# Optimization experiments

Measured on AMD Instinct MI355X. Metric: run time of the kernel, lower is better.

The kernel has to match this reference:

```python
import jax, jax.numpy as jnp
import numpy as np

H = 128
L = 3
N = 100000
E = 1600000
G = 1024
OUT = 10
MAX_LEVEL = 1000
MAX_THOUGHTS = 5000
N_CATE = 5
BN_EPS = 1e-5


def _make_pe(n_pos, h):
    pos = np.arange(n_pos, dtype=np.float32)[:, None]
    div = np.exp(np.arange(0, h, 2, dtype=np.float32) * (-np.log(10000.0) / h))
    pe = np.zeros((n_pos, h), dtype=np.float32)
    pe[:, 0::2] = np.sin(pos * div)
    pe[:, 1::2] = np.cos(pos * div)
    return jnp.asarray(pe)


def setup_inputs() -> dict:
    key = jax.random.key(0)
    ks = jax.random.split(key, 16)
    s = 0.02
    inp = {
        "x": jax.random.randint(ks[0], (N, 3), 0, 5, dtype=jnp.int64 if jax.config.jax_enable_x64 else jnp.int32),
        "edge_index": jax.random.randint(ks[1], (2, E), 0, N),
        "batch": jnp.sort(jax.random.randint(ks[2], (N,), 0, G)),
        "num_graphs": G,
        "pe": _make_pe(MAX_THOUGHTS, H),
        "cate_emb": jax.random.normal(ks[3], (N_CATE, H), jnp.float32) * s,
        "level_emb": jax.random.normal(ks[4], (MAX_LEVEL, H), jnp.float32) * s,
        "conv_W1": jax.random.normal(ks[5], (L, H, H), jnp.float32) * s,
        "conv_b1": jnp.zeros((L, H), jnp.float32),
        "conv_g1": jnp.ones((L, H), jnp.float32),
        "conv_be1": jnp.zeros((L, H), jnp.float32),
        "conv_W2": jax.random.normal(ks[6], (L, H, H), jnp.float32) * s,
        "conv_b2": jnp.zeros((L, H), jnp.float32),
        "norm_g": jnp.ones((L, H), jnp.float32),
        "norm_be": jnp.zeros((L, H), jnp.float32),
        "gate_W1": jax.random.normal(ks[7], (H, H), jnp.float32) * s,
        "gate_b1": jnp.zeros((H,), jnp.float32),
        "gate_W2": jax.random.normal(ks[8], (H, 1), jnp.float32) * s,
        "gate_b2": jnp.zeros((1,), jnp.float32),
        "cls_W1": jax.random.normal(ks[9], (H, H), jnp.float32) * s,
        "cls_b1": jnp.zeros((H,), jnp.float32),
        "cls_g": jnp.ones((H,), jnp.float32),
        "cls_be": jnp.zeros((H,), jnp.float32),
        "cls_W2": jax.random.normal(ks[10], (H, OUT), jnp.float32) * s,
        "cls_b2": jnp.zeros((OUT,), jnp.float32),
    }
    return inp


def _bn(h, g, b):
    # BatchNorm1d, training mode: batch stats over the node/graph dim, biased var
    m = jnp.mean(h, axis=0)
    v = jnp.var(h, axis=0)
    return (h - m) * jax.lax.rsqrt(v + BN_EPS) * g + b


def reference(x, edge_index, batch, num_graphs, pe, cate_emb, level_emb,
              conv_W1, conv_b1, conv_g1, conv_be1, conv_W2, conv_b2,
              norm_g, norm_be, gate_W1, gate_b1, gate_W2, gate_b2,
              cls_W1, cls_b1, cls_g, cls_be, cls_W2, cls_b2):
    # NodeEncoder ('tree'): level + cate + sinusoidal thought PE
    level = jnp.clip(x[:, 0], 0, MAX_LEVEL - 1)
    cate = jnp.clip(x[:, 1], 0, N_CATE - 1)
    thought = jnp.clip(x[:, 2], 0, MAX_THOUGHTS - 1)
    h = cate_emb[cate] + level_emb[level] + pe[thought]  # [N, H]

    src, dst = edge_index[0], edge_index[1]
    n = h.shape[0]
    for i in range(L):
        # GINConv (eps=0): h_i <- MLP(h_i + sum_{j->i} h_j)
        agg = jax.ops.segment_sum(h[src], dst, num_segments=n)
        z = (h + agg) @ conv_W1[i] + conv_b1[i]
        z = jax.nn.relu(_bn(z, conv_g1[i], conv_be1[i]))
        z = z @ conv_W2[i] + conv_b2[i]
        h = jax.nn.relu(_bn(z, norm_g[i], norm_be[i]))

    # GlobalAttention pooling: per-graph softmax over gate scores
    gate = (jax.nn.relu(h @ gate_W1 + gate_b1) @ gate_W2 + gate_b2)[:, 0]  # [N]
    m = jax.ops.segment_max(gate, batch, num_segments=num_graphs)
    e = jnp.exp(gate - m[batch])
    s = jax.ops.segment_sum(e, batch, num_segments=num_graphs)
    alpha = e / s[batch]
    pooled = jax.ops.segment_sum(alpha[:, None] * h, batch, num_segments=num_graphs)  # [G, H]

    # classifier (dropout = 0)
    z = pooled @ cls_W1 + cls_b1
    z = jax.nn.relu(_bn(z, cls_g, cls_be))
    return z @ cls_W2 + cls_b2  # [G, OUT]
```

## Files before the change

kernel.cpp:

```cpp
#include <hip/hip_runtime.h>
#include <math.h>

#define HD 128

typedef __attribute__((ext_vector_type(8))) short bf16x8;
typedef __attribute__((ext_vector_type(8))) unsigned short us8;
typedef __attribute__((ext_vector_type(4))) unsigned short us4;
typedef __attribute__((ext_vector_type(4))) float f32x4;

__device__ __forceinline__ float bf2f(unsigned short u) {
  union { unsigned int i; float f; } v; v.i = ((unsigned int)u) << 16; return v.f;
}
__device__ __forceinline__ unsigned short f2bf(float f) {
  union { float f; unsigned int i; } v; v.f = f;
  unsigned int u = v.i;
  u += 0x7FFFu + ((u >> 16) & 1u);
  return (unsigned short)(u >> 16);
}

__global__ void zero_f(float* p, int n) {
  int i = blockIdx.x * blockDim.x + threadIdx.x;
  if (i < n) p[i] = 0.f;
}

__global__ void zero_int(int* p, int n) {
  int stride = gridDim.x * blockDim.x;
  for (int i = blockIdx.x * blockDim.x + threadIdx.x; i < n; i += stride) p[i] = 0;
}

__global__ void encode_kernel(const int* __restrict__ x, const float* __restrict__ pe,
                              const float* __restrict__ ce, const float* __restrict__ le,
                              float* __restrict__ h, unsigned short* __restrict__ hb, int n) {
  int total = n * HD;
  int stride = gridDim.x * blockDim.x;
  for (int idx = blockIdx.x * blockDim.x + threadIdx.x; idx < total; idx += stride) {
    int node = idx >> 7, c = idx & (HD - 1);
    int lv = x[node * 3 + 0]; lv = lv < 0 ? 0 : (lv > 999 ? 999 : lv);
    int ct = x[node * 3 + 1]; ct = ct < 0 ? 0 : (ct > 4 ? 4 : ct);
    int th = x[node * 3 + 2]; th = th < 0 ? 0 : (th > 4999 ? 4999 : th);
    float v = ce[ct * HD + c] + le[lv * HD + c] + pe[th * HD + c];
    h[idx] = v;
    hb[idx] = f2bf(v);
  }
}

__global__ void prep_w(const float* __restrict__ cW1, const float* __restrict__ cW2,
                       const float* __restrict__ gW1,
                       unsigned short* __restrict__ whi, unsigned short* __restrict__ wlo) {
  int m = blockIdx.x;
  const float* W = (m < 3) ? cW1 + (size_t)m * HD * HD
                 : (m < 6) ? cW2 + (size_t)(m - 3) * HD * HD : gW1;
  unsigned short* oh = whi + (size_t)m * HD * HD;
  unsigned short* ol = wlo + (size_t)m * HD * HD;
  for (int i = threadIdx.x; i < HD * HD; i += 256) {
    int j = i & 7;
    int l = (i >> 3) & 63;
    int p = i >> 9;
    int cg = p >> 2, k4 = p & 3;
    int c = cg * 16 + (l & 15);
    int k = (k4 * 4 + (l >> 4)) * 8 + j;
    float f = W[k * HD + c];
    unsigned short hh = f2bf(f);
    oh[i] = hh;
    ol[i] = f2bf(f - bf2f(hh));
  }
}


__global__ void hist_kernel(const int* __restrict__ ei, int* deg, int E, int Wwin) {
  int pass = blockIdx.x & 7;
  int b = blockIdx.x >> 3;
  int tstride = (gridDim.x >> 3) * blockDim.x;
  for (int e = b * blockDim.x + threadIdx.x; e < E; e += tstride) {
    int d = ei[E + e];
    if (d / Wwin == pass) atomicAdd(&deg[d], 1);
  }
}

#define SCAN_BS 1024
__global__ void scan1_kernel(const int* __restrict__ deg, int* __restrict__ off,
                             int* __restrict__ bsum, int n) {
  __shared__ int sh[256];
  int b = blockIdx.x, t = threadIdx.x;
  int base = b * SCAN_BS + t * 4;
  int v[4];
#pragma unroll
  for (int j = 0; j < 4; j++) v[j] = (base + j < n) ? deg[base + j] : 0;
  int s = v[0] + v[1] + v[2] + v[3];
  sh[t] = s;
  __syncthreads();
  for (int o = 1; o < 256; o <<= 1) {
    int x = (t >= o) ? sh[t - o] : 0;
    __syncthreads();
    sh[t] += x;
    __syncthreads();
  }
  int excl = sh[t] - s;
  if (t == 255) bsum[b] = sh[255];
  int run = excl;
#pragma unroll
  for (int j = 0; j < 4; j++) {
    if (base + j < n) off[base + j] = run;
    run += v[j];
  }
}

__global__ void scan2_kernel(int* bsum, int nb) {
  __shared__ int sh[128];
  int t = threadIdx.x;
  int v = (t < nb) ? bsum[t] : 0;
  sh[t] = v;
  __syncthreads();
  for (int o = 1; o < 128; o <<= 1) {
    int x = (t >= o) ? sh[t - o] : 0;
    __syncthreads();
    sh[t] += x;
    __syncthreads();
  }
  if (t < nb) bsum[t] = sh[t] - v;
}

__global__ void scan3_kernel(int* off, int* cursor, const int* __restrict__ bsum,
                             int n, int E) {
  int idx = blockIdx.x * blockDim.x + threadIdx.x;
  int stride = gridDim.x * blockDim.x;
  for (int i = idx; i < n; i += stride) {
    int v = off[i] + bsum[i >> 10];
    off[i] = v;
    cursor[i] = v;
  }
  if (idx == 0) off[n] = E;
}

__global__ void fill_kernel(const int* __restrict__ ei, int* cursor, int* csr_src,
                            int E, int Wwin) {
  int pass = blockIdx.x & 7;
  int b = blockIdx.x >> 3;
  int tstride = (gridDim.x >> 3) * blockDim.x;
  for (int e = b * blockDim.x + threadIdx.x; e < E; e += tstride) {
    int d = ei[E + e];
    if (d / Wwin == pass) {
      int pos = atomicAdd(&cursor[d], 1);
      csr_src[pos] = ei[e];
    }
  }
}

template<bool BN, bool STATS>
__global__ __launch_bounds__(512, 4)
void gemm_gather(const float* __restrict__ h, const unsigned short* __restrict__ hb,
                 const int* __restrict__ off,
                 const int* __restrict__ src, const float* __restrict__ ab,
                 const unsigned short* __restrict__ Whi,
                 const unsigned short* __restrict__ Wlo,
                 const float* __restrict__ bias, float* __restrict__ outf,
                 float* __restrict__ stat, int Nn) {
  __shared__ unsigned short XsH[128 * HD];
  __shared__ unsigned short XsL[128 * HD];
  __shared__ float red[2 * HD];
  int t = threadIdx.x;
  long rowbase = (long)blockIdx.x * 128;
  int grp = t >> 5, lane = t & 31;

  float4 a4, b4;
  if (BN) {
    a4 = *(const float4*)(ab + lane * 4);
    b4 = *(const float4*)(ab + HD + lane * 4);
  }
#define APPLY_BN(v) if (BN) { \
    v.x = fmaxf(v.x * a4.x + b4.x, 0.f); \
    v.y = fmaxf(v.y * a4.y + b4.y, 0.f); \
    v.z = fmaxf(v.z * a4.z + b4.z, 0.f); \
    v.w = fmaxf(v.w * a4.w + b4.w, 0.f); }
#define UP4(wv) {bf2f(wv[0]), bf2f(wv[1]), bf2f(wv[2]), bf2f(wv[3])}

  for (int rr = 0; rr < 8; rr++) {
    int r = grp + rr * 16;
    long row = rowbase + r; if (row > Nn - 1) row = Nn - 1;
    int s0 = off[row], s1 = off[row + 1];
    float4 acc0 = *(const float4*)(h + row * HD + lane * 4);
    APPLY_BN(acc0);
    float4 acc1 = {0.f, 0.f, 0.f, 0.f};
    float4 acc2 = {0.f, 0.f, 0.f, 0.f};
    float4 acc3 = {0.f, 0.f, 0.f, 0.f};
    int e = s0;
    for (; e + 8 <= s1; e += 8) {
      int i0 = src[e], i1 = src[e + 1], i2 = src[e + 2], i3 = src[e + 3];
      int i4 = src[e + 4], i5 = src[e + 5], i6 = src[e + 6], i7 = src[e + 7];
      us4 w0 = *(const us4*)(hb + (size_t)i0 * HD + lane * 4);
      us4 w1 = *(const us4*)(hb + (size_t)i1 * HD + lane * 4);
      us4 w2 = *(const us4*)(hb + (size_t)i2 * HD + lane * 4);
      us4 w3 = *(const us4*)(hb + (size_t)i3 * HD + lane * 4);
      us4 w4 = *(const us4*)(hb + (size_t)i4 * HD + lane * 4);
      us4 w5 = *(const us4*)(hb + (size_t)i5 * HD + lane * 4);
      us4 w6 = *(const us4*)(hb + (size_t)i6 * HD + lane * 4);
      us4 w7 = *(const us4*)(hb + (size_t)i7 * HD + lane * 4);
      float4 v0 = UP4(w0), v1 = UP4(w1), v2 = UP4(w2), v3 = UP4(w3);
      float4 v4 = UP4(w4), v5 = UP4(w5), v6 = UP4(w6), v7 = UP4(w7);
      APPLY_BN(v0); APPLY_BN(v1); APPLY_BN(v2); APPLY_BN(v3);
      APPLY_BN(v4); APPLY_BN(v5); APPLY_BN(v6); APPLY_BN(v7);
      acc0.x += v0.x + v4.x; acc0.y += v0.y + v4.y; acc0.z += v0.z + v4.z; acc0.w += v0.w + v4.w;
      acc1.x += v1.x + v5.x; acc1.y += v1.y + v5.y; acc1.z += v1.z + v5.z; acc1.w += v1.w + v5.w;
      acc2.x += v2.x + v6.x; acc2.y += v2.y + v6.y; acc2.z += v2.z + v6.z; acc2.w += v2.w + v6.w;
      acc3.x += v3.x + v7.x; acc3.y += v3.y + v7.y; acc3.z += v3.z + v7.z; acc3.w += v3.w + v7.w;
    }
    for (; e < s1; e++) {
      int s = src[e];
      us4 wv = *(const us4*)(hb + (size_t)s * HD + lane * 4);
      float4 v = UP4(wv);
      APPLY_BN(v);
      acc0.x += v.x; acc0.y += v.y; acc0.z += v.z; acc0.w += v.w;
    }
    acc0.x += acc1.x + acc2.x + acc3.x;
    acc0.y += acc1.y + acc2.y + acc3.y;
    acc0.z += acc1.z + acc2.z + acc3.z;
    acc0.w += acc1.w + acc2.w + acc3.w;
    float f[4] = {acc0.x, acc0.y, acc0.z, acc0.w};
    us4 hi, lo;
#pragma unroll
    for (int j = 0; j < 4; j++) {
      unsigned short hh = f2bf(f[j]);
      hi[j] = hh;
      lo[j] = f2bf(f[j] - bf2f(hh));
    }
    int g8 = lane >> 1;
    int offl = r * HD + (((g8 ^ (r & 7)) << 3)) + (lane & 1) * 4;
    *(us4*)(XsH + offl) = hi;
    *(us4*)(XsL + offl) = lo;
  }
#undef APPLY_BN
#undef UP4
  if (STATS && t < 2 * HD) red[t] = 0.f;
  __syncthreads();

  int w = t >> 6, l = t & 63;
  int lr = l & 15, lg = l >> 4;

  f32x4 acc[8];
#pragma unroll
  for (int ct = 0; ct < 8; ct++) acc[ct] = (f32x4){0.f, 0.f, 0.f, 0.f};

  bf16x8 aH[4], aL[4];
  int arow = w * 16 + lr;
#pragma unroll
  for (int k4 = 0; k4 < 4; k4++) {
    int kg = k4 * 4 + lg;
    int offa = arow * HD + (((kg ^ (arow & 7)) << 3));
    aH[k4] = *(bf16x8*)(XsH + offa);
    aL[k4] = *(bf16x8*)(XsL + offa);
  }
#pragma unroll
  for (int ct = 0; ct < 8; ct++) {
#pragma unroll
    for (int k4 = 0; k4 < 4; k4++) {
      int bo = (((ct << 2) + k4) * 64 + l) * 8;
      bf16x8 bH = *(const bf16x8*)(Whi + bo);
      bf16x8 bL = *(const bf16x8*)(Wlo + bo);
      acc[ct] = __builtin_amdgcn_mfma_f32_16x16x32_bf16(aH[k4], bH, acc[ct], 0, 0, 0);
      acc[ct] = __builtin_amdgcn_mfma_f32_16x16x32_bf16(aH[k4], bL, acc[ct], 0, 0, 0);
      acc[ct] = __builtin_amdgcn_mfma_f32_16x16x32_bf16(aL[k4], bH, acc[ct], 0, 0, 0);
    }
  }

  float s[8], ss[8];
#pragma unroll
  for (int ct = 0; ct < 8; ct++) { s[ct] = 0.f; ss[ct] = 0.f; }
#pragma unroll
  for (int jj = 0; jj < 4; jj++) {
    long row = rowbase + w * 16 + lg * 4 + jj;
    bool ok = row < Nn;
#pragma unroll
    for (int ct = 0; ct < 8; ct++) {
      float v = acc[ct][jj] + bias[ct * 16 + lr];
      if (ok) {
        outf[row * HD + ct * 16 + lr] = v;
        if (STATS) { s[ct] += v; ss[ct] += v * v; }
      }
    }
  }
  if (STATS) {
#pragma unroll
    for (int ct = 0; ct < 8; ct++) {
      float sv = s[ct], sq = ss[ct];
      sv += __shfl_xor(sv, 16); sq += __shfl_xor(sq, 16);
      sv += __shfl_xor(sv, 32); sq += __shfl_xor(sq, 32);
      if (lg == 0) {
        atomicAdd(&red[ct * 16 + lr], sv);
        atomicAdd(&red[HD + ct * 16 + lr], sq);
      }
    }
    __syncthreads();
    float* st = stat + (blockIdx.x & 3) * 256;
    if (t < 2 * HD) atomicAdd(&st[t], red[t]);
  }
}

template<bool INBN, bool GATE, bool STATS>
__global__ __launch_bounds__(512, 8)
void gemm_split(const float* __restrict__ X, const unsigned short* __restrict__ Whi,
                const unsigned short* __restrict__ Wlo,
                const float* __restrict__ bias, const float* __restrict__ ab,
                const float* __restrict__ w2, float* __restrict__ outf,
                unsigned short* __restrict__ outb,
                float* __restrict__ gate, float* __restrict__ stat, int Nn) {
  __shared__ unsigned short XsH[64 * HD];
  __shared__ unsigned short XsL[64 * HD];
  __shared__ float red[2 * HD];
  __shared__ float gred[64];
  int t = threadIdx.x;
  long rowbase = (long)blockIdx.x * 64;

#pragma unroll
  for (int it = 0; it < 4; it++) {
    int i = (t + it * 512) * 4;
    int r = i >> 7, k = i & (HD - 1);
    long row = rowbase + r; if (row > Nn - 1) row = Nn - 1;
    float4 v = *(const float4*)(X + row * HD + k);
    float f[4] = {v.x, v.y, v.z, v.w};
    if (INBN) {
#pragma unroll
      for (int j = 0; j < 4; j++)
        f[j] = fmaxf(f[j] * ab[k + j] + ab[HD + k + j], 0.f);
    }
    us4 hi, lo;
#pragma unroll
    for (int j = 0; j < 4; j++) {
      unsigned short hh = f2bf(f[j]);
      hi[j] = hh;
      lo[j] = f2bf(f[j] - bf2f(hh));
    }
    int g = k >> 3;
    int off = r * HD + ((((g ^ (r & 7)) << 3)) | (k & 7));
    *(us4*)(XsH + off) = hi;
    *(us4*)(XsL + off) = lo;
  }
  if (STATS && t < 2 * HD) red[t] = 0.f;
  if (GATE && t < 64) gred[t] = 0.f;
  __syncthreads();

  int w = t >> 6, l = t & 63;
  int lr = l & 15, lg = l >> 4;
  int wr = w & 3, wc = w >> 2;

  f32x4 acc[4];
#pragma unroll
  for (int ct = 0; ct < 4; ct++) acc[ct] = (f32x4){0.f, 0.f, 0.f, 0.f};

  bf16x8 aH[4], aL[4];
  int arow = wr * 16 + lr;
#pragma unroll
  for (int k4 = 0; k4 < 4; k4++) {
    int kg = k4 * 4 + lg;
    int off = arow * HD + (((kg ^ (arow & 7)) << 3));
    aH[k4] = *(bf16x8*)(XsH + off);
    aL[k4] = *(bf16x8*)(XsL + off);
  }
#pragma unroll
  for (int ct = 0; ct < 4; ct++) {
    int cg = wc * 4 + ct;
#pragma unroll
    for (int k4 = 0; k4 < 4; k4++) {
      int bo = (((cg << 2) + k4) * 64 + l) * 8;
      bf16x8 bH = *(const bf16x8*)(Whi + bo);
      bf16x8 bL = *(const bf16x8*)(Wlo + bo);
      acc[ct] = __builtin_amdgcn_mfma_f32_16x16x32_bf16(aH[k4], bH, acc[ct], 0, 0, 0);
      acc[ct] = __builtin_amdgcn_mfma_f32_16x16x32_bf16(aH[k4], bL, acc[ct], 0, 0, 0);
      acc[ct] = __builtin_amdgcn_mfma_f32_16x16x32_bf16(aL[k4], bH, acc[ct], 0, 0, 0);
    }
  }

  if (GATE) {
#pragma unroll
    for (int jj = 0; jj < 4; jj++) {
      float p = 0.f;
#pragma unroll
      for (int ct = 0; ct < 4; ct++) {
        int col = (wc * 4 + ct) * 16 + lr;
        float v = fmaxf(acc[ct][jj] + bias[col], 0.f);
        p += v * w2[col];
      }
      p += __shfl_xor(p, 1);
      p += __shfl_xor(p, 2);
      p += __shfl_xor(p, 4);
      p += __shfl_xor(p, 8);
      if (lr == 0) atomicAdd(&gred[wr * 16 + lg * 4 + jj], p);
    }
    __syncthreads();
    if (t < 64 && rowbase + t < Nn) gate[rowbase + t] = gred[t];
  } else {
    float s[4], ss[4];
#pragma unroll
    for (int ct = 0; ct < 4; ct++) { s[ct] = 0.f; ss[ct] = 0.f; }
#pragma unroll
    for (int jj = 0; jj < 4; jj++) {
      long row = rowbase + wr * 16 + lg * 4 + jj;
      bool ok = row < Nn;
#pragma unroll
      for (int ct = 0; ct < 4; ct++) {
        int col = (wc * 4 + ct) * 16 + lr;
        float v = acc[ct][jj] + bias[col];
        if (ok) {
          outf[row * HD + col] = v;
          if (outb) outb[row * HD + col] = f2bf(v);
          if (STATS) { s[ct] += v; ss[ct] += v * v; }
        }
      }
    }
    if (STATS) {
#pragma unroll
      for (int ct = 0; ct < 4; ct++) {
        int col = (wc * 4 + ct) * 16 + lr;
        float sv = s[ct], sq = ss[ct];
        sv += __shfl_xor(sv, 16); sq += __shfl_xor(sq, 16);
        sv += __shfl_xor(sv, 32); sq += __shfl_xor(sq, 32);
        if (lg == 0) {
          atomicAdd(&red[col], sv);
          atomicAdd(&red[HD + col], sq);
        }
      }
      __syncthreads();
      float* st = stat + (blockIdx.x & 3) * 256;
      if (t < 2 * HD) atomicAdd(&st[t], red[t]);
    }
  }
}

__global__ void finalize_kernel(const float* __restrict__ stat, const float* __restrict__ g,
                                const float* __restrict__ be, float* ab, float inv_n) {
  int c = threadIdx.x;
  float s = stat[c] + stat[256 + c] + stat[512 + c] + stat[768 + c];
  float sq = stat[HD + c] + stat[256 + HD + c] + stat[512 + HD + c] + stat[768 + HD + c];
  float mean = s * inv_n;
  float var = sq * inv_n - mean * mean;
  float inv = rsqrtf(var + 1e-5f);
  float a = inv * g[c];
  ab[c] = a;
  ab[HD + c] = be[c] - mean * a;
}

__global__ void finalize1_kernel(const float* __restrict__ stat, const float* __restrict__ g,
                                 const float* __restrict__ be, float* ab, float inv_n) {
  int c = threadIdx.x;
  float mean = stat[c] * inv_n;
  float var = stat[HD + c] * inv_n - mean * mean;
  float inv = rsqrtf(var + 1e-5f);
  float a = inv * g[c];
  ab[c] = a;
  ab[HD + c] = be[c] - mean * a;
}

__global__ void bound_kernel(const int* __restrict__ batch, int* gs, int N, int G) {
  int i = blockIdx.x * blockDim.x + threadIdx.x;
  if (i >= N) return;
  int b = batch[i];
  int prev = (i == 0) ? -1 : batch[i - 1];
  for (int g = prev + 1; g <= b; g++) gs[g] = i;
  if (i == N - 1)
    for (int g = b + 1; g <= G; g++) gs[g] = N;
}

__global__ void fused_pool(const float* __restrict__ h, const float* __restrict__ gate,
                           const int* __restrict__ gs, const float* __restrict__ ab,
                           float* __restrict__ pooled) {
  int g = blockIdx.x;
  int t = threadIdx.x;
  int s0 = gs[g], s1 = gs[g + 1];
  if (s0 >= s1) { pooled[(size_t)g * HD + t] = 0.f; return; }
  __shared__ float red[HD];
  float m = -INFINITY;
  for (int i = s0 + t; i < s1; i += HD) m = fmaxf(m, gate[i]);
  red[t] = m;
  __syncthreads();
  for (int o = 64; o > 0; o >>= 1) {
    if (t < o) red[t] = fmaxf(red[t], red[t + o]);
    __syncthreads();
  }
  m = red[0];
  __syncthreads();
  float s = 0.f;
  for (int i = s0 + t; i < s1; i += HD) s += expf(gate[i] - m);
  red[t] = s;
  __syncthreads();
  for (int o = 64; o > 0; o >>= 1) {
    if (t < o) red[t] += red[t + o];
    __syncthreads();
  }
  float inv = 1.f / red[0];
  float a = ab[t], b = ab[HD + t];
  float acc = 0.f;
  int i = s0;
  for (; i + 4 <= s1; i += 4) {
    float al0 = expf(gate[i] - m);
    float al1 = expf(gate[i + 1] - m);
    float al2 = expf(gate[i + 2] - m);
    float al3 = expf(gate[i + 3] - m);
    float v0 = fmaxf(h[(size_t)(i + 0) * HD + t] * a + b, 0.f);
    float v1 = fmaxf(h[(size_t)(i + 1) * HD + t] * a + b, 0.f);
    float v2 = fmaxf(h[(size_t)(i + 2) * HD + t] * a + b, 0.f);
    float v3 = fmaxf(h[(size_t)(i + 3) * HD + t] * a + b, 0.f);
    acc += al0 * v0 + al1 * v1 + al2 * v2 + al3 * v3;
  }
  for (; i < s1; i++) {
    float al = expf(gate[i] - m);
    float v = fmaxf(h[(size_t)i * HD + t] * a + b, 0.f);
    acc += al * v;
  }
  pooled[(size_t)g * HD + t] = acc * inv;
}

__global__ __launch_bounds__(256, 4)
void gemm_f32(const float* __restrict__ X, const float* __restrict__ W,
              const float* __restrict__ bias, float* __restrict__ out, int Nn) {
  __shared__ float XsT[32][132];
  __shared__ float Ws[32][HD];
  int t = threadIdx.x;
  int r0 = (t >> 4) * 8;
  int c0 = (t & 15) * 8;
  long rowbase = (long)blockIdx.x * 128;

  float acc[8][8];
#pragma unroll
  for (int ci = 0; ci < 8; ci++) {
    float bv = bias[c0 + ci];
#pragma unroll
    for (int ri = 0; ri < 8; ri++) acc[ri][ci] = bv;
  }

  int sr = t >> 1;
  int hf = t & 1;
  long srow = rowbase + sr; if (srow > Nn - 1) srow = Nn - 1;
  const float* xrow = X + srow * HD;

  for (int k0 = 0; k0 < HD; k0 += 32) {
    __syncthreads();
#pragma unroll
    for (int j = 0; j < 4; j++) {
      int i = j * 1024 + t * 4;
      int kk = i >> 7, c = i & (HD - 1);
      *(float4*)&Ws[kk][c] = *(const float4*)&W[(size_t)(k0 + kk) * HD + c];
    }
#pragma unroll
    for (int j = 0; j < 4; j++) {
      int kc = k0 + hf * 16 + j * 4;
      float4 v = *(const float4*)&xrow[kc];
      int kl = hf * 16 + j * 4;
      XsT[kl + 0][sr] = v.x;
      XsT[kl + 1][sr] = v.y;
      XsT[kl + 2][sr] = v.z;
      XsT[kl + 3][sr] = v.w;
    }
    __syncthreads();
#pragma unroll 8
    for (int kk = 0; kk < 32; kk++) {
      float4 a0 = *(float4*)&XsT[kk][r0];
      float4 a1 = *(float4*)&XsT[kk][r0 + 4];
      float4 b0 = *(float4*)&Ws[kk][c0];
      float4 b1 = *(float4*)&Ws[kk][c0 + 4];
      float ar[8] = {a0.x, a0.y, a0.z, a0.w, a1.x, a1.y, a1.z, a1.w};
      float bc[8] = {b0.x, b0.y, b0.z, b0.w, b1.x, b1.y, b1.z, b1.w};
#pragma unroll
      for (int ri = 0; ri < 8; ri++)
#pragma unroll
        for (int ci = 0; ci < 8; ci++) acc[ri][ci] += ar[ri] * bc[ci];
    }
  }

#pragma unroll
  for (int ri = 0; ri < 8; ri++) {
    long row = rowbase + r0 + ri;
    if (row < Nn) {
      float4 o0 = {acc[ri][0], acc[ri][1], acc[ri][2], acc[ri][3]};
      float4 o1 = {acc[ri][4], acc[ri][5], acc[ri][6], acc[ri][7]};
      *(float4*)&out[row * HD + c0] = o0;
      *(float4*)&out[row * HD + c0 + 4] = o1;
    }
  }
}

__global__ void stats_f32(const float* __restrict__ z, float* stat, int n) {
  int c = threadIdx.x & (HD - 1);
  int rg = threadIdx.x >> 7;
  float s = 0.f, ss = 0.f;
  for (int r = blockIdx.x * 2 + rg; r < n; r += gridDim.x * 2) {
    float v = z[(size_t)r * HD + c];
    s += v; ss += v * v;
  }
  __shared__ float S[2][HD], SS[2][HD];
  S[rg][c] = s; SS[rg][c] = ss;
  __syncthreads();
  if (threadIdx.x < HD) {
    atomicAdd(&stat[c], S[0][c] + S[1][c]);
    atomicAdd(&stat[HD + c], SS[0][c] + SS[1][c]);
  }
}

__global__ void cls_out_kernel(const float* __restrict__ zc, const float* __restrict__ ab,
                               const float* __restrict__ W2, const float* __restrict__ b2,
                               float* out, int G) {
  int row = blockIdx.x;
  int t = threadIdx.x;
  float v0 = fmaxf(zc[(size_t)row * HD + t] * ab[t] + ab[HD + t], 0.f);
  float v1 = fmaxf(zc[(size_t)row * HD + 64 + t] * ab[64 + t] + ab[HD + 64 + t], 0.f);
  for (int o = 0; o < 10; o++) {
    float p = v0 * W2[t * 10 + o] + v1 * W2[(64 + t) * 10 + o];
#pragma unroll
    for (int s = 32; s > 0; s >>= 1) p += __shfl_down(p, s);
    if (t == 0) out[row * 10 + o] = p + b2[o];
  }
}

extern "C" void kernel_launch(void* const* d_in, const int* in_sizes, int n_in,
                              void* d_out, int out_size, void* d_ws, size_t ws_size,
                              hipStream_t stream) {
  const int* x     = (const int*)d_in[0];
  const int* ei    = (const int*)d_in[1];
  const int* batch = (const int*)d_in[2];
  const float* pe  = (const float*)d_in[4];
  const float* ce  = (const float*)d_in[5];
  const float* le  = (const float*)d_in[6];
  const float* cW1 = (const float*)d_in[7];
  const float* cb1 = (const float*)d_in[8];
  const float* cg1 = (const float*)d_in[9];
  const float* cbe1= (const float*)d_in[10];
  const float* cW2 = (const float*)d_in[11];
  const float* cb2 = (const float*)d_in[12];
  const float* ngm = (const float*)d_in[13];
  const float* nbe = (const float*)d_in[14];
  const float* gW1 = (const float*)d_in[15];
  const float* gb1 = (const float*)d_in[16];
  const float* gW2 = (const float*)d_in[17];
  const float* clW1= (const float*)d_in[19];
  const float* clb1= (const float*)d_in[20];
  const float* clg = (const float*)d_in[21];
  const float* clbe= (const float*)d_in[22];
  const float* clW2= (const float*)d_in[23];
  const float* clb2= (const float*)d_in[24];

  int N = in_sizes[2];
  int E = in_sizes[1] / 2;
  int G = out_size / 10;

  float* buf0   = (float*)d_ws;
  float* buf1   = buf0 + (size_t)N * HD;
  float* pooled = buf1 + (size_t)N * HD;
  float* gate   = pooled + (size_t)G * HD;
  float* zc     = gate + N;
  float* stats  = zc + (size_t)G * HD;
  float* ab     = stats + 7 * 1024;
  unsigned short* whi = (unsigned short*)(ab + 7 * 256);
  unsigned short* wlo = whi + 7 * HD * HD;
  unsigned short* hbb = wlo + 7 * HD * HD;
  int* csr_off  = (int*)(hbb + (size_t)N * HD);
  int* cursor   = csr_off + (N + 1);
  int* bsum     = cursor + N;
  int* gs       = bsum + 128;
  int* csr_src  = gs + (G + 1);

  float* out = (float*)d_out;
  int gatherBlocks = (N + 127) / 128;
  int splitBlocks  = (N + 63) / 64;
  int Wwin = (N + 7) / 8;

  zero_f<<<28, 256, 0, stream>>>(stats, 7 * 1024);
  encode_kernel<<<2048, 256, 0, stream>>>(x, pe, ce, le, buf0, hbb, N);
  prep_w<<<7, 256, 0, stream>>>(cW1, cW2, gW1, whi, wlo);

  int nb = (N + SCAN_BS - 1) / SCAN_BS;
  zero_int<<<256, 256, 0, stream>>>(cursor, N);
  hist_kernel<<<2048, 256, 0, stream>>>(ei, cursor, E, Wwin);
  scan1_kernel<<<nb, 256, 0, stream>>>(cursor, csr_off, bsum, N);
  scan2_kernel<<<1, 128, 0, stream>>>(bsum, nb);
  scan3_kernel<<<256, 256, 0, stream>>>(csr_off, cursor, bsum, N, E);
  fill_kernel<<<2048, 256, 0, stream>>>(ei, cursor, csr_src, E, Wwin);
  bound_kernel<<<(N + 255) / 256, 256, 0, stream>>>(batch, gs, N, G);

  for (int l = 0; l < 3; l++) {
    float* abPrev = ab + (l - 1) * 512 + 256;
    if (l == 0)
      gemm_gather<false, true><<<gatherBlocks, 512, 0, stream>>>(
          buf0, hbb, csr_off, csr_src, nullptr,
          whi + (size_t)l * HD * HD, wlo + (size_t)l * HD * HD,
          cb1 + l * HD, buf1, stats + l * 2048, N);
    else
      gemm_gather<true, true><<<gatherBlocks, 512, 0, stream>>>(
          buf0, hbb, csr_off, csr_src, abPrev,
          whi + (size_t)l * HD * HD, wlo + (size_t)l * HD * HD,
          cb1 + l * HD, buf1, stats + l * 2048, N);
    finalize_kernel<<<1, 128, 0, stream>>>(stats + l * 2048, cg1 + l * HD, cbe1 + l * HD,
                                           ab + l * 512, 1.f / N);
    gemm_split<true, false, true><<<splitBlocks, 512, 0, stream>>>(
        buf1, whi + (size_t)(3 + l) * HD * HD, wlo + (size_t)(3 + l) * HD * HD,
        cb2 + l * HD, ab + l * 512, nullptr, buf0, (l < 2) ? hbb : nullptr,
        nullptr, stats + l * 2048 + 1024, N);
    finalize_kernel<<<1, 128, 0, stream>>>(stats + l * 2048 + 1024, ngm + l * HD, nbe + l * HD,
                                           ab + l * 512 + 256, 1.f / N);
  }

  const float* abFin = ab + 2 * 512 + 256;
  gemm_split<true, true, false><<<splitBlocks, 512, 0, stream>>>(
      buf0, whi + (size_t)6 * HD * HD, wlo + (size_t)6 * HD * HD,
      gb1, abFin, gW2, nullptr, nullptr, gate, nullptr, N);
  fused_pool<<<G, HD, 0, stream>>>(buf0, gate, gs, abFin, pooled);

  gemm_f32<<<(G + 127) / 128, 256, 0, stream>>>(pooled, clW1, clb1, zc, G);
  stats_f32<<<64, 256, 0, stream>>>(zc, stats + 6 * 1024, G);
  finalize1_kernel<<<1, 128, 0, stream>>>(stats + 6 * 1024, clg, clbe, ab + 6 * 256, 1.f / G);
  cls_out_kernel<<<G, 64, 0, stream>>>(zc, ab + 6 * 256, clW2, clb2, out, G);
}
```

Before: 774.3 us.

## Fold BatchNorm finalize into consumer kernels and shrink gather tile to 96 rows

Removes the separate single-block finalize kernels by having each consumer kernel (gather GEMM, split GEMM, pooling, classifier output) compute the BatchNorm scale and shift from the raw stats in its prologue. This saves seven tiny launches and their serialization gaps. Separately, the gather GEMM tile drops from 128 to 96 rows with launch bounds raised from 4 to 6 blocks, to cut LDS use and raise occupancy. Two of the eight waves now sit idle during the MFMA phase, and the stats math is repeated in every block.

```diff
diff --git a/kernel.cpp b/kernel.cpp
--- a/kernel.cpp
+++ b/kernel.cpp
@@ -4,7 +4,6 @@
 #define HD 128
 
 typedef __attribute__((ext_vector_type(8))) short bf16x8;
-typedef __attribute__((ext_vector_type(8))) unsigned short us8;
 typedef __attribute__((ext_vector_type(4))) unsigned short us4;
 typedef __attribute__((ext_vector_type(4))) float f32x4;
 
@@ -16,6 +15,18 @@
   unsigned int u = v.i;
   u += 0x7FFFu + ((u >> 16) & 1u);
   return (unsigned short)(u >> 16);
+}
+
+__device__ __forceinline__ void bn_ab(const float* __restrict__ st, const float* __restrict__ g,
+                                      const float* __restrict__ be, float inv_n, int c,
+                                      float& a, float& b) {
+  float s = st[c] + st[256 + c] + st[512 + c] + st[768 + c];
+  float sq = st[HD + c] + st[256 + HD + c] + st[512 + HD + c] + st[768 + HD + c];
+  float mean = s * inv_n;
+  float var = sq * inv_n - mean * mean;
+  float inv = rsqrtf(var + 1e-5f);
+  a = inv * g[c];
+  b = be[c] - mean * a;
 }
 
 __global__ void zero_f(float* p, int n) {
@@ -147,25 +158,37 @@
 }
 
 template<bool BN, bool STATS>
-__global__ __launch_bounds__(512, 4)
+__global__ __launch_bounds__(512, 6)
 void gemm_gather(const float* __restrict__ h, const unsigned short* __restrict__ hb,
-                 const int* __restrict__ off,
-                 const int* __restrict__ src, const float* __restrict__ ab,
+                 const int* __restrict__ off, const int* __restrict__ src,
+                 const float* __restrict__ statP, const float* __restrict__ gBN,
+                 const float* __restrict__ beBN, float inv_n,
                  const unsigned short* __restrict__ Whi,
                  const unsigned short* __restrict__ Wlo,
                  const float* __restrict__ bias, float* __restrict__ outf,
-                 float* __restrict__ stat, int Nn) {
-  __shared__ unsigned short XsH[128 * HD];
-  __shared__ unsigned short XsL[128 * HD];
+                 float* __restrict__ statOut, int Nn) {
+  __shared__ unsigned short XsH[96 * HD];
+  __shared__ unsigned short XsL[96 * HD];
   __shared__ float red[2 * HD];
+  __shared__ float abl[2 * HD];
   int t = threadIdx.x;
-  long rowbase = (long)blockIdx.x * 128;
+  long rowbase = (long)blockIdx.x * 96;
   int grp = t >> 5, lane = t & 31;
+
+  if (BN) {
+    if (t < HD) {
+      float a, b;
+      bn_ab(statP, gBN, beBN, inv_n, t, a, b);
+      abl[t] = a;
+      abl[HD + t] = b;
+    }
+    __syncthreads();
+  }
 
   float4 a4, b4;
   if (BN) {
-    a4 = *(const float4*)(ab + lane * 4);
-    b4 = *(const float4*)(ab + HD + lane * 4);
+    a4 = *(const float4*)(abl + lane * 4);
+    b4 = *(const float4*)(abl + HD + lane * 4);
   }
 #define APPLY_BN(v) if (BN) { \
     v.x = fmaxf(v.x * a4.x + b4.x, 0.f); \
@@ -174,7 +197,7 @@
     v.w = fmaxf(v.w * a4.w + b4.w, 0.f); }
 #define UP4(wv) {bf2f(wv[0]), bf2f(wv[1]), bf2f(wv[2]), bf2f(wv[3])}
 
-  for (int rr = 0; rr < 8; rr++) {
+  for (int rr = 0; rr < 6; rr++) {
     int r = grp + rr * 16;
     long row = rowbase + r; if (row > Nn - 1) row = Nn - 1;
     int s0 = off[row], s1 = off[row + 1];
@@ -236,61 +259,65 @@
   int w = t >> 6, l = t & 63;
   int lr = l & 15, lg = l >> 4;
 
-  f32x4 acc[8];
-#pragma unroll
-  for (int ct = 0; ct < 8; ct++) acc[ct] = (f32x4){0.f, 0.f, 0.f, 0.f};
-
-  bf16x8 aH[4], aL[4];
-  int arow = w * 16 + lr;
-#pragma unroll
-  for (int k4 = 0; k4 < 4; k4++) {
-    int kg = k4 * 4 + lg;
-    int offa = arow * HD + (((kg ^ (arow & 7)) << 3));
-    aH[k4] = *(bf16x8*)(XsH + offa);
-    aL[k4] = *(bf16x8*)(XsL + offa);
-  }
-#pragma unroll
-  for (int ct = 0; ct < 8; ct++) {
+  if (w < 6) {
+    f32x4 acc[8];
+#pragma unroll
+    for (int ct = 0; ct < 8; ct++) acc[ct] = (f32x4){0.f, 0.f, 0.f, 0.f};
+
+    bf16x8 aH[4], aL[4];
+    int arow = w * 16 + lr;
 #pragma unroll
     for (int k4 = 0; k4 < 4; k4++) {
-      int bo = (((ct << 2) + k4) * 64 + l) * 8;
-      bf16x8 bH = *(const bf16x8*)(Whi + bo);
-      bf16x8 bL = *(const bf16x8*)(Wlo + bo);
-      acc[ct] = __builtin_amdgcn_mfma_f32_16x16x32_bf16(aH[k4], bH, acc[ct], 0, 0, 0);
-      acc[ct] = __builtin_amdgcn_mfma_f32_16x16x32_bf16(aH[k4], bL, acc[ct], 0, 0, 0);
-      acc[ct] = __builtin_amdgcn_mfma_f32_16x16x32_bf16(aL[k4], bH, acc[ct], 0, 0, 0);
-    }
-  }
-
-  float s[8], ss[8];
-#pragma unroll
-  for (int ct = 0; ct < 8; ct++) { s[ct] = 0.f; ss[ct] = 0.f; }
-#pragma unroll
-  for (int jj = 0; jj < 4; jj++) {
-    long row = rowbase + w * 16 + lg * 4 + jj;
-    bool ok = row < Nn;
+      int kg = k4 * 4 + lg;
+      int offa = arow * HD + (((kg ^ (arow & 7)) << 3));
+      aH[k4] = *(bf16x8*)(XsH + offa);
+      aL[k4] = *(bf16x8*)(XsL + offa);
+    }
 #pragma unroll
     for (int ct = 0; ct < 8; ct++) {
-      float v = acc[ct][jj] + bias[ct * 16 + lr];
-      if (ok) {
-        outf[row * HD + ct * 16 + lr] = v;
-        if (STATS) { s[ct] += v; ss[ct] += v * v; }
+#pragma unroll
+      for (int k4 = 0; k4 < 4; k4++) {
+        int bo = (((ct << 2) + k4) * 64 + l) * 8;
+        bf16x8 bH = *(const bf16x8*)(Whi + bo);
+        bf16x8 bL = *(const bf16x8*)(Wlo + bo);
+        acc[ct] = __builtin_amdgcn_mfma_f32_16x16x32_bf16(aH[k4], bH, acc[ct], 0, 0, 0);
+        acc[ct] = __builtin_amdgcn_mfma_f32_16x16x32_bf16(aH[k4], bL, acc[ct], 0, 0, 0);
+        acc[ct] = __builtin_amdgcn_mfma_f32_16x16x32_bf16(aL[k4], bH, acc[ct], 0, 0, 0);
       }
     }
+
+    float s[8], ss[8];
+#pragma unroll
+    for (int ct = 0; ct < 8; ct++) { s[ct] = 0.f; ss[ct] = 0.f; }
+#pragma unroll
+    for (int jj = 0; jj < 4; jj++) {
+      long row = rowbase + w * 16 + lg * 4 + jj;
+      bool ok = row < Nn;
+#pragma unroll
+      for (int ct = 0; ct < 8; ct++) {
+        float v = acc[ct][jj] + bias[ct * 16 + lr];
+        if (ok) {
+          outf[row * HD + ct * 16 + lr] = v;
+          if (STATS) { s[ct] += v; ss[ct] += v * v; }
+        }
+      }
+    }
+    if (STATS) {
+#pragma unroll
+      for (int ct = 0; ct < 8; ct++) {
+        float sv = s[ct], sq = ss[ct];
+        sv += __shfl_xor(sv, 16); sq += __shfl_xor(sq, 16);
+        sv += __shfl_xor(sv, 32); sq += __shfl_xor(sq, 32);
+        if (lg == 0) {
+          atomicAdd(&red[ct * 16 + lr], sv);
+          atomicAdd(&red[HD + ct * 16 + lr], sq);
+        }
+      }
+    }
   }
   if (STATS) {
-#pragma unroll
-    for (int ct = 0; ct < 8; ct++) {
-      float sv = s[ct], sq = ss[ct];
-      sv += __shfl_xor(sv, 16); sq += __shfl_xor(sq, 16);
-      sv += __shfl_xor(sv, 32); sq += __shfl_xor(sq, 32);
-      if (lg == 0) {
-        atomicAdd(&red[ct * 16 + lr], sv);
-        atomicAdd(&red[HD + ct * 16 + lr], sq);
-      }
-    }
-    __syncthreads();
-    float* st = stat + (blockIdx.x & 3) * 256;
+    __syncthreads();
+    float* st = statOut + (blockIdx.x & 3) * 256;
     if (t < 2 * HD) atomicAdd(&st[t], red[t]);
   }
 }
@@ -299,16 +326,31 @@
 __global__ __launch_bounds__(512, 8)
 void gemm_split(const float* __restrict__ X, const unsigned short* __restrict__ Whi,
                 const unsigned short* __restrict__ Wlo,
-                const float* __restrict__ bias, const float* __restrict__ ab,
+                const float* __restrict__ bias,
+                const float* __restrict__ statP, const float* __restrict__ gBN,
+                const float* __restrict__ beBN, float inv_n,
                 const float* __restrict__ w2, float* __restrict__ outf,
                 unsigned short* __restrict__ outb,
-                float* __restrict__ gate, float* __restrict__ stat, int Nn) {
+                float* __restrict__ gate, float* __restrict__ statOut, int Nn) {
   __shared__ unsigned short XsH[64 * HD];
   __shared__ unsigned short XsL[64 * HD];
   __shared__ float red[2 * HD];
   __shared__ float gred[64];
+  __shared__ float abl[2 * HD];
   int t = threadIdx.x;
   long rowbase = (long)blockIdx.x * 64;
+
+  if (INBN) {
+    if (t < HD) {
+      float a, b;
+      bn_ab(statP, gBN, beBN, inv_n, t, a, b);
+      abl[t] = a;
+      abl[HD + t] = b;
+    }
+  }
+  if (STATS && t < 2 * HD) red[t] = 0.f;
+  if (GATE && t < 64) gred[t] = 0.f;
+  if (INBN) __syncthreads();
 
 #pragma unroll
   for (int it = 0; it < 4; it++) {
@@ -320,7 +362,7 @@
     if (INBN) {
 #pragma unroll
       for (int j = 0; j < 4; j++)
-        f[j] = fmaxf(f[j] * ab[k + j] + ab[HD + k + j], 0.f);
+        f[j] = fmaxf(f[j] * abl[k + j] + abl[HD + k + j], 0.f);
     }
     us4 hi, lo;
 #pragma unroll
@@ -334,8 +376,6 @@
     *(us4*)(XsH + off) = hi;
     *(us4*)(XsL + off) = lo;
   }
-  if (STATS && t < 2 * HD) red[t] = 0.f;
-  if (GATE && t < 64) gred[t] = 0.f;
   __syncthreads();
 
   int w = t >> 6, l = t & 63;
@@ -419,34 +459,10 @@
         }
       }
       __syncthreads();
-      float* st = stat + (blockIdx.x & 3) * 256;
+      float* st = statOut + (blockIdx.x & 3) * 256;
       if (t < 2 * HD) atomicAdd(&st[t], red[t]);
     }
   }
-}
-
-__global__ void finalize_kernel(const float* __restrict__ stat, const float* __restrict__ g,
-                                const float* __restrict__ be, float* ab, float inv_n) {
-  int c = threadIdx.x;
-  float s = stat[c] + stat[256 + c] + stat[512 + c] + stat[768 + c];
-  float sq = stat[HD + c] + stat[256 + HD + c] + stat[512 + HD + c] + stat[768 + HD + c];
-  float mean = s * inv_n;
-  float var = sq * inv_n - mean * mean;
-  float inv = rsqrtf(var + 1e-5f);
-  float a = inv * g[c];
-  ab[c] = a;
-  ab[HD + c] = be[c] - mean * a;
-}
-
-__global__ void finalize1_kernel(const float* __restrict__ stat, const float* __restrict__ g,
-                                 const float* __restrict__ be, float* ab, float inv_n) {
-  int c = threadIdx.x;
-  float mean = stat[c] * inv_n;
-  float var = stat[HD + c] * inv_n - mean * mean;
-  float inv = rsqrtf(var + 1e-5f);
-  float a = inv * g[c];
-  ab[c] = a;
-  ab[HD + c] = be[c] - mean * a;
 }
 
 __global__ void bound_kernel(const int* __restrict__ batch, int* gs, int N, int G) {
@@ -460,13 +476,17 @@
 }
 
 __global__ void fused_pool(const float* __restrict__ h, const float* __restrict__ gate,
-                           const int* __restrict__ gs, const float* __restrict__ ab,
+                           const int* __restrict__ gs,
+                           const float* __restrict__ statP, const float* __restrict__ gBN,
+                           const float* __restrict__ beBN, float inv_n,
                            float* __restrict__ pooled) {
   int g = blockIdx.x;
   int t = threadIdx.x;
   int s0 = gs[g], s1 = gs[g + 1];
   if (s0 >= s1) { pooled[(size_t)g * HD + t] = 0.f; return; }
   __shared__ float red[HD];
+  float a, b;
+  bn_ab(statP, gBN, beBN, inv_n, t, a, b);
   float m = -INFINITY;
   for (int i = s0 + t; i < s1; i += HD) m = fmaxf(m, gate[i]);
   red[t] = m;
@@ -486,7 +506,6 @@
     __syncthreads();
   }
   float inv = 1.f / red[0];
-  float a = ab[t], b = ab[HD + t];
   float acc = 0.f;
   int i = s0;
   for (; i + 4 <= s1; i += 4) {
@@ -594,13 +613,22 @@
   }
 }
 
-__global__ void cls_out_kernel(const float* __restrict__ zc, const float* __restrict__ ab,
-                               const float* __restrict__ W2, const float* __restrict__ b2,
-                               float* out, int G) {
+__global__ void cls_out_kernel(const float* __restrict__ zc, const float* __restrict__ stat,
+                               const float* __restrict__ g, const float* __restrict__ be,
+                               float inv_n, const float* __restrict__ W2,
+                               const float* __restrict__ b2, float* out, int G) {
   int row = blockIdx.x;
   int t = threadIdx.x;
-  float v0 = fmaxf(zc[(size_t)row * HD + t] * ab[t] + ab[HD + t], 0.f);
-  float v1 = fmaxf(zc[(size_t)row * HD + 64 + t] * ab[64 + t] + ab[HD + 64 + t], 0.f);
+  float mean0 = stat[t] * inv_n;
+  float var0 = stat[HD + t] * inv_n - mean0 * mean0;
+  float a0 = rsqrtf(var0 + 1e-5f) * g[t];
+  float b0 = be[t] - mean0 * a0;
+  float mean1 = stat[64 + t] * inv_n;
+  float var1 = stat[HD + 64 + t] * inv_n - mean1 * mean1;
+  float a1 = rsqrtf(var1 + 1e-5f) * g[64 + t];
+  float b1 = be[64 + t] - mean1 * a1;
+  float v0 = fmaxf(zc[(size_t)row * HD + t] * a0 + b0, 0.f);
+  float v1 = fmaxf(zc[(size_t)row * HD + 64 + t] * a1 + b1, 0.f);
   for (int o = 0; o < 10; o++) {
     float p = v0 * W2[t * 10 + o] + v1 * W2[(64 + t) * 10 + o];
 #pragma unroll
@@ -646,8 +674,7 @@
   float* gate   = pooled + (size_t)G * HD;
   float* zc     = gate + N;
   float* stats  = zc + (size_t)G * HD;
-  float* ab     = stats + 7 * 1024;
-  unsigned short* whi = (unsigned short*)(ab + 7 * 256);
+  unsigned short* whi = (unsigned short*)(stats + 7 * 1024);
   unsigned short* wlo = whi + 7 * HD * HD;
   unsigned short* hbb = wlo + 7 * HD * HD;
   int* csr_off  = (int*)(hbb + (size_t)N * HD);
@@ -657,9 +684,10 @@
   int* csr_src  = gs + (G + 1);
 
   float* out = (float*)d_out;
-  int gatherBlocks = (N + 127) / 128;
+  int gatherBlocks = (N + 95) / 96;
   int splitBlocks  = (N + 63) / 64;
   int Wwin = (N + 7) / 8;
+  float invN = 1.f / N;
 
   zero_f<<<28, 256, 0, stream>>>(stats, 7 * 1024);
   encode_kernel<<<2048, 256, 0, stream>>>(x, pe, ce, le, buf0, hbb, N);
@@ -675,35 +703,33 @@
   bound_kernel<<<(N + 255) / 256, 256, 0, stream>>>(batch, gs, N, G);
 
   for (int l = 0; l < 3; l++) {
-    float* abPrev = ab + (l - 1) * 512 + 256;
+    const float* statPrev = stats + (l - 1) * 2048 + 1024;
     if (l == 0)
       gemm_gather<false, true><<<gatherBlocks, 512, 0, stream>>>(
-          buf0, hbb, csr_off, csr_src, nullptr,
+          buf0, hbb, csr_off, csr_src, nullptr, nullptr, nullptr, invN,
           whi + (size_t)l * HD * HD, wlo + (size_t)l * HD * HD,
           cb1 + l * HD, buf1, stats + l * 2048, N);
     else
       gemm_gather<true, true><<<gatherBlocks, 512, 0, stream>>>(
-          buf0, hbb, csr_off, csr_src, abPrev,
+          buf0, hbb, csr_off, csr_src, statPrev, ngm + (l - 1) * HD, nbe + (l - 1) * HD, invN,
           whi + (size_t)l * HD * HD, wlo + (size_t)l * HD * HD,
           cb1 + l * HD, buf1, stats + l * 2048, N);
-    finalize_kernel<<<1, 128, 0, stream>>>(stats + l * 2048, cg1 + l * HD, cbe1 + l * HD,
-                                           ab + l * 512, 1.f / N);
     gemm_split<true, false, true><<<splitBlocks, 512, 0, stream>>>(
         buf1, whi + (size_t)(3 + l) * HD * HD, wlo + (size_t)(3 + l) * HD * HD,
-        cb2 + l * HD, ab + l * 512, nullptr, buf0, (l < 2) ? hbb : nullptr,
-        nullptr, stats + l * 2048 + 1024, N);
-    finalize_kernel<<<1, 128, 0, stream>>>(stats + l * 2048 + 1024, ngm + l * HD, nbe + l * HD,
-                                           ab + l * 512 + 256, 1.f / N);
-  }
-
-  const float* abFin = ab + 2 * 512 + 256;
+        cb2 + l * HD, stats + l * 2048, cg1 + l * HD, cbe1 + l * HD, invN,
+        nullptr, buf0, (l < 2) ? hbb : nullptr, nullptr, stats + l * 2048 + 1024, N);
+  }
+
+  const float* statFin = stats + 2 * 2048 + 1024;
   gemm_split<true, true, false><<<splitBlocks, 512, 0, stream>>>(
       buf0, whi + (size_t)6 * HD * HD, wlo + (size_t)6 * HD * HD,
-      gb1, abFin, gW2, nullptr, nullptr, gate, nullptr, N);
-  fused_pool<<<G, HD, 0, stream>>>(buf0, gate, gs, abFin, pooled);
+      gb1, statFin, ngm + 2 * HD, nbe + 2 * HD, invN,
+      gW2, nullptr, nullptr, gate, nullptr, N);
+  fused_pool<<<G, HD, 0, stream>>>(buf0, gate, gs, statFin, ngm + 2 * HD, nbe + 2 * HD,
+                                   invN, pooled);
 
   gemm_f32<<<(G + 127) / 128, 256, 0, stream>>>(pooled, clW1, clb1, zc, G);
   stats_f32<<<64, 256, 0, stream>>>(zc, stats + 6 * 1024, G);
-  finalize1_kernel<<<1, 128, 0, stream>>>(stats + 6 * 1024, clg, clbe, ab + 6 * 256, 1.f / G);
-  cls_out_kernel<<<G, 64, 0, stream>>>(zc, ab + 6 * 256, clW2, clb2, out, G);
-}
+  cls_out_kernel<<<G, 64, 0, stream>>>(zc, stats + 6 * 1024, clg, clbe, 1.f / G,
+                                       clW2, clb2, out, G);
+}
```

New measurement: 756.5 us. 1.02x faster.
